# Kernel optimization log

Measured on AMD Instinct MI355X. Metric: run time of the kernel, lower is better.

The kernel has to match this reference:

```python
import jax, jax.numpy as jnp
import numpy as np

HEADS = 8
LANDMARKS = 256
PINV_ITERS = 6
KSZ = 33          # res_conv kernel size (lucidrains default)
LN_EPS = 1e-5


def setup_inputs() -> dict:
    key = jax.random.key(0)
    ks = jax.random.split(key, 5)
    b, n, d = 4, 8192, 512
    inner = 512  # heads * dim_head = 8 * 64
    s = 0.02
    return {
        "x": jax.random.normal(ks[0], (b, n, d), jnp.float32),
        "ln_w": jnp.ones((d,), jnp.float32),
        "ln_b": jnp.zeros((d,), jnp.float32),
        "w_qkv": jax.random.normal(ks[1], (3 * inner, d), jnp.float32) * s,  # Linear(d, 3*inner, bias=False)
        "w_out": jax.random.normal(ks[2], (d, inner), jnp.float32) * s,      # Linear(inner, d)
        "b_out": jnp.zeros((d,), jnp.float32),
        "conv_w": jax.random.normal(ks[3], (HEADS, 1, KSZ, 1), jnp.float32) * 0.1,  # depthwise Conv2d(h,h,(33,1),groups=h)
    }


def _pinv(x, iters):
    # Moore-Penrose iterative pseudo-inverse (lucidrains)
    abs_x = jnp.abs(x)
    scale = jnp.max(abs_x.sum(-1)) * jnp.max(abs_x.sum(-2))
    z = jnp.swapaxes(x, -1, -2) / scale
    I = jnp.eye(x.shape[-1], dtype=x.dtype)
    for _ in range(iters):
        xz = x @ z
        z = 0.25 * z @ (13.0 * I - xz @ (15.0 * I - xz @ (7.0 * I - xz)))
    return z


def _forward(x, ln_w, ln_b, w_qkv, w_out, b_out, conv_w):
    b, n, d = x.shape
    h, m = HEADS, LANDMARKS
    dh = d // h  # 64
    # --- LayerNorm ---
    mu = jnp.mean(x, -1, keepdims=True)
    var = jnp.var(x, -1, keepdims=True)
    xn = (x - mu) / jnp.sqrt(var + LN_EPS) * ln_w + ln_b
    # --- qkv ---
    qkv = xn @ w_qkv.T
    q, k, v = jnp.split(qkv, 3, axis=-1)
    to_heads = lambda t: t.reshape(b, n, h, dh).transpose(0, 2, 1, 3)  # b h n dh
    q = to_heads(q) * (dh ** -0.5)
    k = to_heads(k)
    v = to_heads(v)
    # --- landmarks: mean over contiguous groups of length l (einops '(n l) d -> n d') ---
    l = n // m
    q_l = q.reshape(b, h, m, l, dh).mean(3)  # b h m dh
    k_l = k.reshape(b, h, m, l, dh).mean(3)
    # --- three softmax attention matrices ---
    attn1 = jax.nn.softmax(jnp.einsum('bhid,bhjd->bhij', q, k_l), -1)    # b h n m
    attn2 = jax.nn.softmax(jnp.einsum('bhid,bhjd->bhij', q_l, k_l), -1)  # b h m m
    attn3 = jax.nn.softmax(jnp.einsum('bhid,bhjd->bhij', q_l, k), -1)    # b h m n
    out = (attn1 @ _pinv(attn2, PINV_ITERS)) @ (attn3 @ v)               # b h n dh
    # --- residual depthwise conv over sequence dim, per head, shared over dh ---
    pad = KSZ // 2
    res = jax.lax.conv_general_dilated(
        v, conv_w, window_strides=(1, 1), padding=[(pad, pad), (0, 0)],
        dimension_numbers=('NCHW', 'OIHW', 'NCHW'), feature_group_count=h)
    out = out + res
    out = out.transpose(0, 2, 1, 3).reshape(b, n, h * dh)
    attn_out = out @ w_out.T + b_out  # dropout is identity in eval
    return x + attn_out  # TransLayer residual


def reference(x, ln_w, ln_b, w_qkv, w_out, b_out, conv_w):
    return _forward(x, ln_w, ln_b, w_qkv, w_out, b_out, conv_w)
```

## Files before the change

kernel.cpp:

```cpp
#include <hip/hip_runtime.h>

typedef unsigned short u16;
typedef unsigned int u32;
typedef __attribute__((ext_vector_type(8))) short bf16x8;
typedef __attribute__((ext_vector_type(4))) float f32x4;

__device__ __forceinline__ float bf2f(u16 u) {
    union { u32 i; float f; } z; z.i = ((u32)u) << 16; return z.f;
}
__device__ __forceinline__ float bflo(u32 w) {
    union { u32 i; float f; } z; z.i = w << 16; return z.f;
}
__device__ __forceinline__ float bfhi(u32 w) {
    union { u32 i; float f; } z; z.i = w & 0xffff0000u; return z.f;
}
__device__ __forceinline__ u16 f2bf(float f) {
    union { float f; u32 i; } z; z.f = f;
    u32 x = z.i;
    return (u16)((x + 0x7FFFu + ((x >> 16) & 1u)) >> 16);
}
__device__ __forceinline__ u32 pack2bf(float a, float b) {
    return (u32)f2bf(a) | ((u32)f2bf(b) << 16);
}
template<int BF>
__device__ __forceinline__ float ldin(const void* p, size_t i) {
    return BF ? bf2f(((const u16*)p)[i]) : ((const float*)p)[i];
}


__global__ void detect_dtype(const void* lnw, int* flg) {
    if (threadIdx.x == 0 && blockIdx.x == 0) {
        u32 w = *(const u32*)lnw;
        *flg = (w == 0x3F803F80u) ? 1 : 0;
    }
}

__global__ __launch_bounds__(256) void conv2bf(const void* src, u16* dst, int count, const int* flg) {
    int idx = (blockIdx.x * 256 + threadIdx.x) * 4;
    if (idx >= count) return;
    if (*flg) {
        *(ulonglong1*)&dst[idx] = *(const ulonglong1*)&((const u16*)src)[idx];
    } else {
        const float* s = (const float*)src;
        u32 p0 = pack2bf(s[idx], s[idx + 1]);
        u32 p1 = pack2bf(s[idx + 2], s[idx + 3]);
        *(uint2*)&dst[idx] = make_uint2(p0, p1);
    }
}

template<int BF>
__device__ __forceinline__ void ln_row(const void* x, const void* lnw, const void* lnb, u16* xn) {
    int lane = threadIdx.x & 63;
    size_t row = (size_t)blockIdx.x * 4 + (threadIdx.x >> 6);
    size_t base = row * 512;
    float v[8];
    if (BF) {
        uint4 u = ((const uint4*)((const u16*)x + base))[lane];
        u32 wd[4] = {u.x, u.y, u.z, u.w};
#pragma unroll
        for (int e = 0; e < 4; e++) { v[2 * e] = bflo(wd[e]); v[2 * e + 1] = bfhi(wd[e]); }
    } else {
        const float4* xp = (const float4*)((const float*)x + base) + 2 * lane;
        float4 a = xp[0], b = xp[1];
        v[0] = a.x; v[1] = a.y; v[2] = a.z; v[3] = a.w;
        v[4] = b.x; v[5] = b.y; v[6] = b.z; v[7] = b.w;
    }
    float s = 0.f, s2 = 0.f;
#pragma unroll
    for (int e = 0; e < 8; e++) { s += v[e]; s2 += v[e] * v[e]; }
#pragma unroll
    for (int m = 1; m < 64; m <<= 1) { s += __shfl_xor(s, m); s2 += __shfl_xor(s2, m); }
    float mu = s * (1.f / 512.f);
    float var = s2 * (1.f / 512.f) - mu * mu;
    float rstd = rsqrtf(var + 1e-5f);
    float wv[8], bv[8];
    if (BF) {
        uint4 uw = ((const uint4*)lnw)[lane];
        uint4 ub = ((const uint4*)lnb)[lane];
        u32 ww[4] = {uw.x, uw.y, uw.z, uw.w};
        u32 bb[4] = {ub.x, ub.y, ub.z, ub.w};
#pragma unroll
        for (int e = 0; e < 4; e++) {
            wv[2 * e] = bflo(ww[e]); wv[2 * e + 1] = bfhi(ww[e]);
            bv[2 * e] = bflo(bb[e]); bv[2 * e + 1] = bfhi(bb[e]);
        }
    } else {
        const float4* wp = (const float4*)lnw + 2 * lane;
        const float4* bp = (const float4*)lnb + 2 * lane;
        float4 w0 = wp[0], w1 = wp[1], b0 = bp[0], b1 = bp[1];
        wv[0] = w0.x; wv[1] = w0.y; wv[2] = w0.z; wv[3] = w0.w;
        wv[4] = w1.x; wv[5] = w1.y; wv[6] = w1.z; wv[7] = w1.w;
        bv[0] = b0.x; bv[1] = b0.y; bv[2] = b0.z; bv[3] = b0.w;
        bv[4] = b1.x; bv[5] = b1.y; bv[6] = b1.z; bv[7] = b1.w;
    }
    uint4 o;
    u32 ow[4];
#pragma unroll
    for (int e = 0; e < 4; e++) {
        float f0 = (v[2 * e] - mu) * rstd * wv[2 * e] + bv[2 * e];
        float f1 = (v[2 * e + 1] - mu) * rstd * wv[2 * e + 1] + bv[2 * e + 1];
        ow[e] = pack2bf(f0, f1);
    }
    o.x = ow[0]; o.y = ow[1]; o.z = ow[2]; o.w = ow[3];
    ((uint4*)(xn + base))[lane] = o;
}
__global__ __launch_bounds__(256) void ln_fused(
    const void* x, const void* lnw, const void* lnb, u16* xn, const int* flg) {
    if (*flg) ln_row<1>(x, lnw, lnb, xn);
    else      ln_row<0>(x, lnw, lnb, xn);
}

__global__ __launch_bounds__(256) void mfma_gemm_qkv(
    const u16* __restrict__ A, const u16* __restrict__ B,
    u16* __restrict__ qp, u16* __restrict__ kp, u16* __restrict__ vp)
{
    __shared__ u16 Asl[128][40];
    __shared__ u16 Bsl[128][40];
    int t = threadIdx.x;
    int wave = t >> 6, lane = t & 63;
    int bid = blockIdx.y * 12 + blockIdx.x;
    int w = (bid & 7) * 384 + (bid >> 3);
    int col0 = (w % 12) * 128, row0 = (w / 12) * 128;
    int wr = (wave & 1) * 64, wc = (wave >> 1) * 64;
    int lrow = lane & 15, koff = (lane >> 4) * 8;
    f32x4 acc[4][4] = {};
    int srow = t >> 2, sch = (t & 3) * 8;
    for (int k0 = 0; k0 < 512; k0 += 32) {
        *(float4*)&Asl[srow][sch]      = *(const float4*)&A[(size_t)(row0 + srow) * 512 + k0 + sch];
        *(float4*)&Asl[srow + 64][sch] = *(const float4*)&A[(size_t)(row0 + srow + 64) * 512 + k0 + sch];
        *(float4*)&Bsl[srow][sch]      = *(const float4*)&B[(size_t)(col0 + srow) * 512 + k0 + sch];
        *(float4*)&Bsl[srow + 64][sch] = *(const float4*)&B[(size_t)(col0 + srow + 64) * 512 + k0 + sch];
        __syncthreads();
        bf16x8 af[4], bfr[4];
#pragma unroll
        for (int i = 0; i < 4; i++) af[i]  = *(const bf16x8*)&Asl[wr + 16 * i + lrow][koff];
#pragma unroll
        for (int j = 0; j < 4; j++) bfr[j] = *(const bf16x8*)&Bsl[wc + 16 * j + lrow][koff];
#pragma unroll
        for (int i = 0; i < 4; i++)
#pragma unroll
            for (int j = 0; j < 4; j++)
                acc[i][j] = __builtin_amdgcn_mfma_f32_16x16x32_bf16(af[i], bfr[j], acc[i][j], 0, 0, 0);
        __syncthreads();
    }
    int crow = (lane >> 4) * 4, ccol = lane & 15;
#pragma unroll
    for (int i = 0; i < 4; i++) {
#pragma unroll
        for (int j = 0; j < 4; j++) {
#pragma unroll
            for (int rg = 0; rg < 4; rg++) {
                int row = row0 + wr + 16 * i + crow + rg;
                int col = col0 + wc + 16 * j + ccol;
                int bi = row >> 13, ii = row & 8191;
                int which = col >> 9, wi = col & 511, hh = wi >> 6, cc = wi & 63;
                size_t dst = (((size_t)bi * 8 + hh) * 8192 + ii) * 64 + cc;
                float v = acc[i][j][rg];
                if (which == 0)      qp[dst] = f2bf(v * 0.125f);
                else if (which == 1) kp[dst] = f2bf(v);
                else                 vp[dst] = f2bf(v);
            }
        }
    }
}

__global__ __launch_bounds__(256) void landmark_kernel(
    const u16* __restrict__ q, const u16* __restrict__ k,
    float* __restrict__ q_l, float* __restrict__ k_l,
    u16* __restrict__ q_l_bf, u16* __restrict__ k_l_bf)
{
    int bh = blockIdx.x;
    int g = blockIdx.y * 4 + (threadIdx.x >> 6);
    int c = threadIdx.x & 63;
    const u16* src = blockIdx.z ? k : q;
    float* dst = blockIdx.z ? k_l : q_l;
    u16* dstbf = blockIdx.z ? k_l_bf : q_l_bf;
    const u16* p0 = src + (((size_t)bh * 8192) + (size_t)g * 32) * 64 + c;
    float s = 0.f;
#pragma unroll
    for (int il = 0; il < 32; il++) s += bf2f(p0[(size_t)il * 64]);
    float mean = s * (1.f / 32.f);
    dst[((size_t)bh * 256 + g) * 64 + c] = mean;
    dstbf[((size_t)bh * 256 + g) * 64 + c] = f2bf(mean);
}

__global__ __launch_bounds__(256) void attn2_kernel(
    const float* __restrict__ q_l, const float* __restrict__ k_l, float* __restrict__ attn2)
{
    int bh = blockIdx.x, i = blockIdx.y, j = threadIdx.x;
    __shared__ float qrow[64];
    __shared__ float red[256];
    if (j < 64) qrow[j] = q_l[((size_t)bh * 256 + i) * 64 + j];
    __syncthreads();
    const float* kb = k_l + ((size_t)bh * 256 + j) * 64;
    float s = 0.f;
#pragma unroll
    for (int c = 0; c < 64; c++) s += qrow[c] * kb[c];
    red[j] = s; __syncthreads();
    for (int off = 128; off; off >>= 1) { if (j < off) red[j] = fmaxf(red[j], red[j + off]); __syncthreads(); }
    float mx = red[0]; __syncthreads();
    float e = __expf(s - mx);
    red[j] = e; __syncthreads();
    for (int off = 128; off; off >>= 1) { if (j < off) red[j] += red[j + off]; __syncthreads(); }
    attn2[((size_t)bh * 256 + i) * 256 + j] = e / red[0];
}

__global__ void init_scale(float* s) {
    if (threadIdx.x == 0) { s[0] = 1.0f; s[1] = 0.f; }
}

__global__ __launch_bounds__(256) void colmax_kernel(const float* __restrict__ X, float* __restrict__ scl)
{
    int bh = blockIdx.x, t = threadIdx.x;
    const float* Xb = X + (size_t)bh * 65536;
    float cs = 0.f;
    for (int i = 0; i < 256; i++) cs += fabsf(Xb[(size_t)i * 256 + t]);
    __shared__ float red[256];
    red[t] = cs; __syncthreads();
    for (int off = 128; off; off >>= 1) { if (t < off) red[t] = fmaxf(red[t], red[t + off]); __syncthreads(); }
    if (t == 0) atomicMax((u32*)&scl[1], __float_as_uint(red[0]));
}

__global__ __launch_bounds__(256) void zinit_p(
    const float* __restrict__ X, const float* __restrict__ scl,
    u16* __restrict__ Zh, u16* __restrict__ Zl)
{
    __shared__ float tile[64][65];
    int b = blockIdx.x;
    int j0 = blockIdx.y * 64, i0 = blockIdx.z * 64;
    float s = scl[0] * scl[1];
    const float* Xb = X + (size_t)b * 65536;
    int t = threadIdx.x;
#pragma unroll
    for (int p = 0; p < 16; p++) {
        int idx = t + 256 * p; int jj = idx >> 6, ii = idx & 63;
        tile[jj][ii] = Xb[(size_t)(j0 + jj) * 256 + i0 + ii];
    }
    __syncthreads();
#pragma unroll
    for (int p = 0; p < 16; p++) {
        int idx = t + 256 * p; int ii = idx >> 6, jj = idx & 63;
        float v = tile[jj][ii] / s;
        u16 hi = f2bf(v);
        u16 lo = f2bf(v - bf2f(hi));
        size_t o = ((size_t)b * 256 + i0 + ii) * 256 + j0 + jj;
        Zh[o] = hi; Zl[o] = lo;
    }
}

__global__ __launch_bounds__(256) void split_at2(
    const float* __restrict__ src, u16* __restrict__ dh, u16* __restrict__ dl)
{
    int idx = (blockIdx.x * 256 + threadIdx.x) * 4;
    float4 v = *(const float4*)&src[idx];
    ushort4 h, l;
    h.x = f2bf(v.x); l.x = f2bf(v.x - bf2f(h.x));
    h.y = f2bf(v.y); l.y = f2bf(v.y - bf2f(h.y));
    h.z = f2bf(v.z); l.z = f2bf(v.z - bf2f(h.z));
    h.w = f2bf(v.w); l.w = f2bf(v.w - bf2f(h.w));
    *(ushort4*)&dh[idx] = h;
    *(ushort4*)&dl[idx] = l;
}

__global__ __launch_bounds__(256) void bmm_fused(
    const float* __restrict__ A, const float* __restrict__ B,
    float* __restrict__ C, float* __restrict__ Cneg,
    int N, float alpha, float cdiag)
{
    int batch = blockIdx.x;
    int row0 = blockIdx.y * 64, col0 = blockIdx.z * 64;
    const float* Ab = A + (size_t)batch * 256 * 256;
    const float* Bb = B + (size_t)batch * 256 * N;
    __shared__ float As[32][68];
    __shared__ float Bs[32][68];
    int t = threadIdx.x, tx = t & 15, ty = t >> 4;
    float acc[4][4] = {};
    for (int k0 = 0; k0 < 256; k0 += 32) {
#pragma unroll
        for (int p = 0; p < 8; p++) {
            int idx = t + 256 * p;
            int ra = idx >> 5, ca = idx & 31;
            As[ca][ra] = Ab[(size_t)(row0 + ra) * 256 + k0 + ca];
            int kb = idx >> 6, cb = idx & 63;
            Bs[kb][cb] = Bb[(size_t)(k0 + kb) * N + col0 + cb];
        }
        __syncthreads();
#pragma unroll
        for (int kk = 0; kk < 32; kk++) {
            float4 av = *(const float4*)&As[kk][ty * 4];
            float4 bv = *(const float4*)&Bs[kk][tx * 4];
            float a[4] = {av.x, av.y, av.z, av.w};
            float bb[4] = {bv.x, bv.y, bv.z, bv.w};
#pragma unroll
            for (int i = 0; i < 4; i++)
#pragma unroll
                for (int j = 0; j < 4; j++) acc[i][j] += a[i] * bb[j];
        }
        __syncthreads();
    }
#pragma unroll
    for (int i = 0; i < 4; i++) {
        int row = row0 + ty * 4 + i;
#pragma unroll
        for (int j = 0; j < 4; j++) {
            int col = col0 + tx * 4 + j;
            float v = alpha * acc[i][j];
            size_t idx = (size_t)batch * 256 * N + (size_t)row * N + col;
            if (C)    C[idx] = v;
            if (Cneg) Cneg[idx] = ((row == col) ? cdiag : 0.f) - v;
        }
    }
}

__global__ __launch_bounds__(256) void bmm3p(
    const u16* __restrict__ Ahg, const u16* __restrict__ Alg,
    const u16* __restrict__ Bhg, const u16* __restrict__ Blg,
    u16* __restrict__ Ch, u16* __restrict__ Cl,
    u16* __restrict__ Nh, u16* __restrict__ Nl,
    float* __restrict__ Cf, float alpha, float cdiag)
{
    __shared__ u16 Ah[64][40], Al[64][40], Bh[64][40], Bl[64][40];
    int batch = blockIdx.x;
    int row0 = blockIdx.y * 64, col0 = blockIdx.z * 64;
    size_t boff = (size_t)batch * 65536;
    int t = threadIdx.x, wave = t >> 6, lane = t & 63;
    int lrow = lane & 15, koff = (lane >> 4) * 8;
    int ar = t >> 2, akq = (t & 3) * 8;
    f32x4 acc[4] = {};
    for (int k0 = 0; k0 < 256; k0 += 32) {
        *(uint4*)&Ah[ar][akq] = *(const uint4*)&Ahg[boff + (size_t)(row0 + ar) * 256 + k0 + akq];
        *(uint4*)&Al[ar][akq] = *(const uint4*)&Alg[boff + (size_t)(row0 + ar) * 256 + k0 + akq];
#pragma unroll
        for (int p = 0; p < 2; p++) {
            int c = t + 256 * p; int n = c & 63, kq = (c >> 6) * 4;
            size_t bb = boff + (size_t)(k0 + kq) * 256 + col0 + n;
            ushort4 hv, lv;
            hv.x = Bhg[bb];       lv.x = Blg[bb];
            hv.y = Bhg[bb + 256]; lv.y = Blg[bb + 256];
            hv.z = Bhg[bb + 512]; lv.z = Blg[bb + 512];
            hv.w = Bhg[bb + 768]; lv.w = Blg[bb + 768];
            *(ushort4*)&Bh[n][kq] = hv;
            *(ushort4*)&Bl[n][kq] = lv;
        }
        __syncthreads();
        bf16x8 ah = *(const bf16x8*)&Ah[wave * 16 + lrow][koff];
        bf16x8 al = *(const bf16x8*)&Al[wave * 16 + lrow][koff];
#pragma unroll
        for (int j = 0; j < 4; j++) {
            bf16x8 bhv = *(const bf16x8*)&Bh[16 * j + lrow][koff];
            bf16x8 blv = *(const bf16x8*)&Bl[16 * j + lrow][koff];
            acc[j] = __builtin_amdgcn_mfma_f32_16x16x32_bf16(ah, bhv, acc[j], 0, 0, 0);
            acc[j] = __builtin_amdgcn_mfma_f32_16x16x32_bf16(ah, blv, acc[j], 0, 0, 0);
            acc[j] = __builtin_amdgcn_mfma_f32_16x16x32_bf16(al, bhv, acc[j], 0, 0, 0);
        }
        __syncthreads();
    }
    int crow = (lane >> 4) * 4, ccol = lane & 15;
#pragma unroll
    for (int j = 0; j < 4; j++) {
#pragma unroll
        for (int r = 0; r < 4; r++) {
            int row = row0 + wave * 16 + crow + r;
            int col = col0 + 16 * j + ccol;
            float v = alpha * acc[j][r];
            size_t idx = boff + (size_t)row * 256 + col;
            if (Cf) Cf[idx] = v;
            if (Ch) {
                u16 hi = f2bf(v);
                Ch[idx] = hi; Cl[idx] = f2bf(v - bf2f(hi));
            }
            if (Nh) {
                float w = ((row == col) ? cdiag : 0.f) - v;
                u16 hi = f2bf(w);
                Nh[idx] = hi; Nl[idx] = f2bf(w - bf2f(hi));
            }
        }
    }
}

__global__ __launch_bounds__(256) void t2bf(const float* __restrict__ src, u16* __restrict__ dst)
{
    __shared__ u16 tile[256][72];
    int bh = blockIdx.x, t = threadIdx.x;
    const float* s = src + (size_t)bh * 16384;
    u16* d = dst + (size_t)bh * 16384;
#pragma unroll
    for (int p = 0; p < 64; p++) {
        int idx = t + 256 * p;
        tile[idx >> 6][idx & 63] = f2bf(s[idx]);
    }
    __syncthreads();
#pragma unroll
    for (int p = 0; p < 64; p++) {
        int o = t + 256 * p;
        int n = o >> 8, kk = o & 255;
        d[o] = tile[kk][n];
    }
}

__global__ __launch_bounds__(256) void attn3v_mfma(
    const u16* __restrict__ qlbf, const u16* __restrict__ k, const u16* __restrict__ v,
    float* __restrict__ Opart, float* __restrict__ lpart)
{
    __shared__ __align__(16) char smem[8192 + 8192 + 9216];
    char* QsB = smem;
    char* KsB = smem + 8192;
    char* VtB = smem + 16384;

    int bh = blockIdx.x, rb = blockIdx.y, seg = blockIdx.z;
    int t = threadIdx.x;
    int w = t >> 6, lane = t & 63, cl = lane & 15, kg = lane >> 4;
    int wrow = w * 16;

    {
        const uint4* qg = (const uint4*)(qlbf + ((size_t)bh * 256 + rb * 64) * 64);
#pragma unroll
        for (int p = 0; p < 2; p++) {
            int c = t + 256 * p; int row = c >> 3, cc = c & 7;
            *(uint4*)(QsB + row * 128 + ((cc * 16) ^ ((row & 7) << 4))) = qg[c];
        }
    }
    __syncthreads();
    bf16x8 af0, af1;
    {
        int row = wrow + cl, sw = (row & 7) << 4;
        af0 = *(const bf16x8*)(QsB + row * 128 + ((kg * 16) ^ sw));
        af1 = *(const bf16x8*)(QsB + row * 128 + ((kg * 16 + 64) ^ sw));
    }

    const uint4* kb4 = (const uint4*)(k + (size_t)bh * 8192 * 64);
    const uint4* vb4 = (const uint4*)(v + (size_t)bh * 8192 * 64);

    int krow = t >> 3, kcc = t & 7;
    int pn = t >> 3, vcc = t & 7;

    f32x4 acc_o[4] = {};
    float rsum[4] = {0.f, 0.f, 0.f, 0.f};

    int n0 = seg * 2048;
    uint4 kr0 = kb4[(size_t)(n0 + krow) * 8 + kcc];
    uint4 kr1 = kb4[(size_t)(n0 + krow + 32) * 8 + kcc];
    uint4 va  = vb4[(size_t)(n0 + 2 * pn) * 8 + vcc];
    uint4 vbv = vb4[(size_t)(n0 + 2 * pn + 1) * 8 + vcc];

    for (int ti = 0; ti < 32; ti++) {
        __syncthreads();
        *(uint4*)(KsB + krow * 128 + ((kcc * 16) ^ ((krow & 7) << 4))) = kr0;
        {
            int row = krow + 32;
            *(uint4*)(KsB + row * 128 + ((kcc * 16) ^ ((row & 7) << 4))) = kr1;
        }
        {
            u32 aw[4] = {va.x, va.y, va.z, va.w};
            u32 bw[4] = {vbv.x, vbv.y, vbv.z, vbv.w};
            int colb = pn * 4;
#pragma unroll
            for (int e = 0; e < 8; e++) {
                u32 avv = (aw[e >> 1] >> ((e & 1) * 16)) & 0xffffu;
                u32 bvv = (bw[e >> 1] >> ((e & 1) * 16)) & 0xffffu;
                int row = vcc * 8 + e;
                *(u32*)(VtB + row * 144 + (colb ^ ((row & 0x38) << 1))) = avv | (bvv << 16);
            }
        }
        __syncthreads();
        if (ti < 31) {
            int nn = n0 + (ti + 1) * 64;
            kr0 = kb4[(size_t)(nn + krow) * 8 + kcc];
            kr1 = kb4[(size_t)(nn + krow + 32) * 8 + kcc];
            va  = vb4[(size_t)(nn + 2 * pn) * 8 + vcc];
            vbv = vb4[(size_t)(nn + 2 * pn + 1) * 8 + vcc];
        }
        f32x4 s[4] = {};
#pragma unroll
        for (int j = 0; j < 4; j++) {
            int row = 16 * j + cl, sw = (row & 7) << 4;
            bf16x8 b0 = *(const bf16x8*)(KsB + row * 128 + ((kg * 16) ^ sw));
            bf16x8 b1 = *(const bf16x8*)(KsB + row * 128 + ((kg * 16 + 64) ^ sw));
            s[j] = __builtin_amdgcn_mfma_f32_16x16x32_bf16(af0, b0, s[j], 0, 0, 0);
            s[j] = __builtin_amdgcn_mfma_f32_16x16x32_bf16(af1, b1, s[j], 0, 0, 0);
        }
#pragma unroll
        for (int j = 0; j < 4; j++)
#pragma unroll
            for (int r = 0; r < 4; r++) {
                float e = __expf(s[j][r]);
                s[j][r] = e;
                rsum[r] += e;
            }
#pragma unroll
        for (int j = 0; j < 4; j++) {
#pragma unroll
            for (int r = 0; r < 4; r++) {
                float pv = s[j][r];
                float po = __shfl_xor(pv, 1);
                if (!(cl & 1)) {
                    int row = wrow + kg * 4 + r;
                    int col = 16 * j + cl;
                    *(u32*)(QsB + row * 128 + ((col * 2) ^ ((row & 7) << 4))) = pack2bf(pv, po);
                }
            }
        }
        {
            int prow = wrow + cl, psw = (prow & 7) << 4;
            bf16x8 pa0 = *(const bf16x8*)(QsB + prow * 128 + ((kg * 16) ^ psw));
            bf16x8 pa1 = *(const bf16x8*)(QsB + prow * 128 + ((kg * 16 + 64) ^ psw));
#pragma unroll
            for (int j = 0; j < 4; j++) {
                int vr = 16 * j + cl;
                int vsw = (vr & 0x38) << 1;
                bf16x8 vb0 = *(const bf16x8*)(VtB + vr * 144 + ((kg * 16) ^ vsw));
                bf16x8 vb1 = *(const bf16x8*)(VtB + vr * 144 + ((kg * 16 + 64) ^ vsw));
                acc_o[j] = __builtin_amdgcn_mfma_f32_16x16x32_bf16(pa0, vb0, acc_o[j], 0, 0, 0);
                acc_o[j] = __builtin_amdgcn_mfma_f32_16x16x32_bf16(pa1, vb1, acc_o[j], 0, 0, 0);
            }
        }
    }
#pragma unroll
    for (int j = 0; j < 4; j++)
#pragma unroll
        for (int r = 0; r < 4; r++) {
            int lm = rb * 64 + wrow + kg * 4 + r;
            Opart[(((size_t)(bh * 256 + lm)) * 4 + seg) * 64 + 16 * j + cl] = acc_o[j][r];
        }
#pragma unroll
    for (int m = 1; m < 16; m <<= 1)
#pragma unroll
        for (int r = 0; r < 4; r++) rsum[r] += __shfl_xor(rsum[r], m);
    if (cl == 0) {
#pragma unroll
        for (int r = 0; r < 4; r++)
            lpart[((size_t)(bh * 256 + rb * 64 + wrow + kg * 4 + r)) * 4 + seg] = rsum[r];
    }
}

__global__ __launch_bounds__(256) void merge3(
    const float* __restrict__ Opart, const float* __restrict__ lpart, float* __restrict__ w3v)
{
    size_t idx = (size_t)blockIdx.x * 256 + threadIdx.x;
    size_t row = idx >> 6; int c = (int)(idx & 63);
    float l = lpart[row * 4] + lpart[row * 4 + 1] + lpart[row * 4 + 2] + lpart[row * 4 + 3];
    float ov = 0.f;
#pragma unroll
    for (int s = 0; s < 4; s++) ov += Opart[(row * 4 + s) * 64 + c];
    w3v[idx] = ov / l;
}

__global__ __launch_bounds__(256) void attn1_out_mfma(
    const u16* __restrict__ q, const u16* __restrict__ klbf,
    const u16* __restrict__ tmatT, const u16* __restrict__ v,
    const void* __restrict__ conv_w, u16* __restrict__ out2, const int* flg)
{
    __shared__ __align__(16) char smem[31296];
    char* QsB = smem;
    char* KsB = smem + 8192;
    char* TsB = smem + 16384;
    float* Osm = (float*)smem;
    char* VsB = smem + 17472;
    __shared__ float cw[33];

    int bh = blockIdx.x, rb = blockIdx.y;
    int bi = bh >> 3, h = bh & 7;
    int r0 = rb * 64;
    int t = threadIdx.x;
    int w = t >> 6, lane = t & 63, cl = lane & 15, kg = lane >> 4;
    int wrow = w * 16;

    {
        const uint4* qg = (const uint4*)(q + ((size_t)bh * 8192 + r0) * 64);
#pragma unroll
        for (int p = 0; p < 2; p++) {
            int c = t + 256 * p; int row = c >> 3, cc = c & 7;
            *(uint4*)(QsB + row * 128 + ((cc * 16) ^ ((row & 7) << 4))) = qg[c];
        }
    }
    if (t < 33) cw[t] = (*flg) ? bf2f(((const u16*)conv_w)[h * 33 + t])
                               : ((const float*)conv_w)[h * 33 + t];
    __syncthreads();

    bf16x8 af0, af1;
    {
        int row = wrow + cl, sw = (row & 7) << 4;
        af0 = *(const bf16x8*)(QsB + row * 128 + ((kg * 16) ^ sw));
        af1 = *(const bf16x8*)(QsB + row * 128 + ((kg * 16 + 64) ^ sw));
    }

    const uint4* klg = (const uint4*)(klbf + (size_t)bh * 16384);
    const uint4* tg  = (const uint4*)(tmatT + (size_t)bh * 16384);

    f32x4 accO[4] = {};
    float rsum[4] = {0.f, 0.f, 0.f, 0.f};

    for (int lc = 0; lc < 4; lc++) {
        __syncthreads();
#pragma unroll
        for (int p = 0; p < 2; p++) {
            int c = t + 256 * p; int row = c >> 3, cc = c & 7;
            *(uint4*)(KsB + row * 128 + ((cc * 16) ^ ((row & 7) << 4))) = klg[(size_t)(lc * 64 + row) * 8 + cc];
        }
#pragma unroll
        for (int p = 0; p < 2; p++) {
            int c = t + 256 * p; int n = c >> 3, cc = c & 7;
            *(uint4*)(TsB + n * 128 + ((cc * 16) ^ ((n & 7) << 4))) = tg[(size_t)n * 32 + lc * 8 + cc];
        }
        __syncthreads();
        f32x4 s[4] = {};
#pragma unroll
        for (int j = 0; j < 4; j++) {
            int row = 16 * j + cl, sw = (row & 7) << 4;
            bf16x8 b0 = *(const bf16x8*)(KsB + row * 128 + ((kg * 16) ^ sw));
            bf16x8 b1 = *(const bf16x8*)(KsB + row * 128 + ((kg * 16 + 64) ^ sw));
            s[j] = __builtin_amdgcn_mfma_f32_16x16x32_bf16(af0, b0, s[j], 0, 0, 0);
            s[j] = __builtin_amdgcn_mfma_f32_16x16x32_bf16(af1, b1, s[j], 0, 0, 0);
        }
#pragma unroll
        for (int j = 0; j < 4; j++)
#pragma unroll
            for (int r = 0; r < 4; r++) {
                float e = __expf(s[j][r]);
                s[j][r] = e;
                rsum[r] += e;
            }
#pragma unroll
        for (int j = 0; j < 4; j++) {
#pragma unroll
            for (int r = 0; r < 4; r++) {
                float pv = s[j][r];
                float po = __shfl_xor(pv, 1);
                if (!(cl & 1)) {
                    int row = wrow + kg * 4 + r;
                    int col = 16 * j + cl;
                    *(u32*)(QsB + row * 128 + ((col * 2) ^ ((row & 7) << 4))) = pack2bf(pv, po);
                }
            }
        }
        {
            int prow = wrow + cl, psw = (prow & 7) << 4;
            bf16x8 pa0 = *(const bf16x8*)(QsB + prow * 128 + ((kg * 16) ^ psw));
            bf16x8 pa1 = *(const bf16x8*)(QsB + prow * 128 + ((kg * 16 + 64) ^ psw));
#pragma unroll
            for (int j = 0; j < 4; j++) {
                int n = 16 * j + cl, tsw = (n & 7) << 4;
                bf16x8 b0 = *(const bf16x8*)(TsB + n * 128 + ((kg * 16) ^ tsw));
                bf16x8 b1 = *(const bf16x8*)(TsB + n * 128 + ((kg * 16 + 64) ^ tsw));
                accO[j] = __builtin_amdgcn_mfma_f32_16x16x32_bf16(pa0, b0, accO[j], 0, 0, 0);
                accO[j] = __builtin_amdgcn_mfma_f32_16x16x32_bf16(pa1, b1, accO[j], 0, 0, 0);
            }
        }
    }
#pragma unroll
    for (int m = 1; m < 16; m <<= 1)
#pragma unroll
        for (int r = 0; r < 4; r++) rsum[r] += __shfl_xor(rsum[r], m);
    float linv[4];
#pragma unroll
    for (int r = 0; r < 4; r++) linv[r] = 1.f / rsum[r];
#pragma unroll
    for (int j = 0; j < 4; j++)
#pragma unroll
        for (int r = 0; r < 4; r++) accO[j][r] *= linv[r];

    __syncthreads();
    uint4 vreg[3];
    {
        const uint4* vg = (const uint4*)(v + (size_t)bh * 8192 * 64);
#pragma unroll
        for (int p = 0; p < 3; p++) {
            int c = t + 256 * p; int vr = c >> 3, cc = c & 7;
            int gr = r0 - 16 + vr;
            vreg[p] = (gr >= 0 && gr < 8192) ? vg[(size_t)gr * 8 + cc] : make_uint4(0, 0, 0, 0);
        }
    }
#pragma unroll
    for (int j = 0; j < 4; j++)
#pragma unroll
        for (int r = 0; r < 4; r++)
            Osm[(wrow + kg * 4 + r) * 68 + 16 * j + cl] = accO[j][r];
#pragma unroll
    for (int p = 0; p < 3; p++) {
        int c = t + 256 * p; int vr = c >> 3, cc = c & 7;
        *(uint4*)(VsB + vr * 144 + cc * 16) = vreg[p];
    }
    __syncthreads();
    float cwr[33];
#pragma unroll
    for (int i = 0; i < 33; i++) cwr[i] = cw[i];
    int rgrp = t >> 4, cchunk = t & 15;
    float racc[4][4] = {};
#pragma unroll
    for (int vri = 0; vri < 36; vri++) {
        int vr = rgrp * 4 + vri;
        uint2 vv = *(const uint2*)(VsB + vr * 144 + cchunk * 8);
        float v0 = bflo(vv.x), v1 = bfhi(vv.x), v2 = bflo(vv.y), v3 = bfhi(vv.y);
#pragma unroll
        for (int rr = 0; rr < 4; rr++) {
            int tap = vri - rr;
            if (tap >= 0 && tap < 33) {
                float cwt = cwr[tap];
                racc[rr][0] += cwt * v0;
                racc[rr][1] += cwt * v1;
                racc[rr][2] += cwt * v2;
                racc[rr][3] += cwt * v3;
            }
        }
    }
#pragma unroll
    for (int rr = 0; rr < 4; rr++) {
        int ro = rgrp * 4 + rr;
        float4 ov = *(const float4*)&Osm[ro * 68 + cchunk * 4];
        float f0 = ov.x + racc[rr][0];
        float f1 = ov.y + racc[rr][1];
        float f2 = ov.z + racc[rr][2];
        float f3 = ov.w + racc[rr][3];
        size_t base = ((size_t)bi * 8192 + r0 + ro) * 512 + h * 64 + cchunk * 4;
        *(uint2*)(out2 + base) = make_uint2(pack2bf(f0, f1), pack2bf(f2, f3));
    }
}

__global__ __launch_bounds__(256) void mfma_gemm_out(
    const u16* __restrict__ A, const u16* __restrict__ B,
    const void* __restrict__ bias, const void* __restrict__ x,
    void* __restrict__ out, const int* flg)
{
    __shared__ u16 Asl[128][40];
    __shared__ u16 Bsl[128][40];
    int t = threadIdx.x;
    int wave = t >> 6, lane = t & 63;
    int bid = blockIdx.y * 4 + blockIdx.x;
    int w = (bid & 7) * 128 + (bid >> 3);
    int col0 = (w & 3) * 128, row0 = (w >> 2) * 128;
    int wr = (wave & 1) * 64, wc = (wave >> 1) * 64;
    int lrow = lane & 15, koff = (lane >> 4) * 8;
    f32x4 acc[4][4] = {};
    int srow = t >> 2, sch = (t & 3) * 8;
    for (int k0 = 0; k0 < 512; k0 += 32) {
        *(float4*)&Asl[srow][sch]      = *(const float4*)&A[(size_t)(row0 + srow) * 512 + k0 + sch];
        *(float4*)&Asl[srow + 64][sch] = *(const float4*)&A[(size_t)(row0 + srow + 64) * 512 + k0 + sch];
        *(float4*)&Bsl[srow][sch]      = *(const float4*)&B[(size_t)(col0 + srow) * 512 + k0 + sch];
        *(float4*)&Bsl[srow + 64][sch] = *(const float4*)&B[(size_t)(col0 + srow + 64) * 512 + k0 + sch];
        __syncthreads();
        bf16x8 af[4], bfr[4];
#pragma unroll
        for (int i = 0; i < 4; i++) af[i]  = *(const bf16x8*)&Asl[wr + 16 * i + lrow][koff];
#pragma unroll
        for (int j = 0; j < 4; j++) bfr[j] = *(const bf16x8*)&Bsl[wc + 16 * j + lrow][koff];
#pragma unroll
        for (int i = 0; i < 4; i++)
#pragma unroll
            for (int j = 0; j < 4; j++)
                acc[i][j] = __builtin_amdgcn_mfma_f32_16x16x32_bf16(af[i], bfr[j], acc[i][j], 0, 0, 0);
        __syncthreads();
    }
    int crow = (lane >> 4) * 4, ccol = lane & 15;
    int isbf = *flg;
#pragma unroll
    for (int i = 0; i < 4; i++) {
#pragma unroll
        for (int j = 0; j < 4; j++) {
#pragma unroll
            for (int rg = 0; rg < 4; rg++) {
                int row = row0 + wr + 16 * i + crow + rg;
                int col = col0 + wc + 16 * j + ccol;
                size_t idx = (size_t)row * 512 + col;
                float bv = isbf ? bf2f(((const u16*)bias)[col]) : ((const float*)bias)[col];
                float xv = isbf ? bf2f(((const u16*)x)[idx]) : ((const float*)x)[idx];
                float v = acc[i][j][rg] + bv + xv;
                if (isbf) ((u16*)out)[idx] = f2bf(v);
                else      ((float*)out)[idx] = v;
            }
        }
    }
}

extern "C" void kernel_launch(void* const* d_in, const int* in_sizes, int n_in,
                              void* d_out, int out_size, void* d_ws, size_t ws_size,
                              hipStream_t stream) {
    const void* x      = d_in[0];
    const void* ln_w   = d_in[1];
    const void* ln_b   = d_in[2];
    const void* w_qkv  = d_in[3];
    const void* w_out  = d_in[4];
    const void* b_out  = d_in[5];
    const void* conv_w = d_in[6];

    char* base = (char*)d_ws;
    size_t off = 0;
    auto alloc = [&](size_t nbytes) { char* p = base + off; off += (nbytes + 255) & ~size_t(255); return p; };
    u16*   q_bf  = (u16*)  alloc(16777216ull * 2);
    u16*   k_bf  = (u16*)  alloc(16777216ull * 2);
    u16*   v_bf  = (u16*)  alloc(16777216ull * 2);
    u16*   xn_bf = (u16*)  alloc(16777216ull * 2);
    u16*   wq_bf = (u16*)  alloc(786432ull * 2);
    u16*   wo_bf = (u16*)  alloc(262144ull * 2);
    float* q_l   = (float*)alloc(524288ull * 4);
    float* k_l   = (float*)alloc(524288ull * 4);
    float* at2   = (float*)alloc(2097152ull * 4);
    float* zf32  = (float*)alloc(2097152ull * 4);
    float* Zb    = (float*)alloc(2097152ull * 4);
    float* XZ    = (float*)alloc(2097152ull * 4);
    u16*   T1h   = (u16*)  alloc(2097152ull * 2);
    u16*   T1l   = (u16*)  alloc(2097152ull * 2);
    float* w3v   = (float*)alloc(524288ull * 4);
    float* tmat  = (float*)alloc(524288ull * 4);
    u16*   ql_bf = (u16*)  alloc(524288ull * 2);
    u16*   kl_bf = (u16*)  alloc(524288ull * 2);
    u16*   tmT   = (u16*)  alloc(524288ull * 2);
    float* scl   = (float*)alloc(256);
    int*   flg   = (int*)  alloc(256);

    u16* a2h = xn_bf;
    u16* a2l = xn_bf + 2097152ull;
    u16* Zah = xn_bf + 2097152ull * 2;
    u16* Zal = xn_bf + 2097152ull * 3;
    u16* Zbh = xn_bf + 2097152ull * 4;
    u16* Zbl = xn_bf + 2097152ull * 5;
    u16* XZh = xn_bf + 2097152ull * 6;
    u16* XZl = xn_bf + 2097152ull * 7;

    detect_dtype<<<1, 64, 0, stream>>>(ln_w, flg);
    ln_fused<<<8192, 256, 0, stream>>>(x, ln_w, ln_b, xn_bf, flg);
    conv2bf<<<768, 256, 0, stream>>>(w_qkv, wq_bf, 786432, flg);
    conv2bf<<<256, 256, 0, stream>>>(w_out, wo_bf, 262144, flg);
    mfma_gemm_qkv<<<dim3(12, 256), 256, 0, stream>>>(xn_bf, wq_bf, q_bf, k_bf, v_bf);
    landmark_kernel<<<dim3(32, 64, 2), 256, 0, stream>>>(q_bf, k_bf, q_l, k_l, ql_bf, kl_bf);
    attn2_kernel<<<dim3(32, 256), 256, 0, stream>>>(q_l, k_l, at2);
    init_scale<<<1, 64, 0, stream>>>(scl);
    colmax_kernel<<<32, 256, 0, stream>>>(at2, scl);
    zinit_p<<<dim3(32, 4, 4), 256, 0, stream>>>(at2, scl, Zah, Zal);
    split_at2<<<2048, 256, 0, stream>>>(at2, a2h, a2l);

    u16 *zch = Zah, *zcl = Zal, *znh = Zbh, *znl = Zbl;
    for (int it = 0; it < 6; it++) {
        bmm3p<<<dim3(32, 4, 4), 256, 0, stream>>>(a2h, a2l, zch, zcl, XZh, XZl, T1h, T1l, nullptr, 1.f, 7.f);
        bmm3p<<<dim3(32, 4, 4), 256, 0, stream>>>(XZh, XZl, T1h, T1l, nullptr, nullptr, znh, znl, nullptr, 1.f, 15.f);
        bmm3p<<<dim3(32, 4, 4), 256, 0, stream>>>(XZh, XZl, znh, znl, nullptr, nullptr, T1h, T1l, nullptr, 1.f, 13.f);
        bmm3p<<<dim3(32, 4, 4), 256, 0, stream>>>(zch, zcl, T1h, T1l, znh, znl, nullptr, nullptr,
                                                  (it == 5) ? zf32 : nullptr, 0.25f, 0.f);
        u16* th = zch; zch = znh; znh = th;
        u16* tl = zcl; zcl = znl; znl = tl;
    }
    float* Opart = Zb;
    float* lpart = XZ;

    attn3v_mfma<<<dim3(32, 4, 4), 256, 0, stream>>>(ql_bf, k_bf, v_bf, Opart, lpart);
    merge3<<<2048, 256, 0, stream>>>(Opart, lpart, w3v);
    bmm_fused<<<dim3(32, 4, 1), 256, 0, stream>>>(zf32, w3v, tmat, nullptr, 64, 1.f, 0.f);
    t2bf<<<32, 256, 0, stream>>>(tmat, tmT);
    u16* out2 = k_bf;
    attn1_out_mfma<<<dim3(32, 128), 256, 0, stream>>>(q_bf, kl_bf, tmT, v_bf, conv_w, out2, flg);
    mfma_gemm_out<<<dim3(4, 256), 256, 0, stream>>>(out2, wo_bf, b_out, x, d_out, flg);
}
```

Before: 868.4 us.

## Load full landmark K and T tiles once and remap bmm3p block order

attn1_out_mfma now loads all 256 landmark keys and the full transposed T matrix into 64KB of shared memory in one pass, computes the whole 64x256 score tile in registers, normalizes, then runs one P·T pass. This replaces the four-chunk loop with a barrier pair per chunk. Q fragments are read straight from global memory rather than staged through shared memory. Separately, bmm3p remaps its flat block index so tiles of the same batch are spread across blocks in interleaved order. The 64KB of LDS and 16 accumulator tiles per thread raise register and LDS pressure, which may cut occupancy.

```diff
diff --git a/kernel.cpp b/kernel.cpp
--- a/kernel.cpp
+++ b/kernel.cpp
@@ -320,8 +320,11 @@
     float* __restrict__ Cf, float alpha, float cdiag)
 {
     __shared__ u16 Ah[64][40], Al[64][40], Bh[64][40], Bl[64][40];
-    int batch = blockIdx.x;
-    int row0 = blockIdx.y * 64, col0 = blockIdx.z * 64;
+    int bid = blockIdx.x + 32 * (blockIdx.y + 4 * blockIdx.z);
+    int w = (bid & 7) * 64 + (bid >> 3);
+    int batch = w >> 4;
+    int tile = w & 15;
+    int row0 = (tile >> 2) * 64, col0 = (tile & 3) * 64;
     size_t boff = (size_t)batch * 65536;
     int t = threadIdx.x, wave = t >> 6, lane = t & 63;
     int lrow = lane & 15, koff = (lane >> 4) * 8;
@@ -370,9 +373,9 @@
                 Ch[idx] = hi; Cl[idx] = f2bf(v - bf2f(hi));
             }
             if (Nh) {
-                float w = ((row == col) ? cdiag : 0.f) - v;
-                u16 hi = f2bf(w);
-                Nh[idx] = hi; Nl[idx] = f2bf(w - bf2f(hi));
+                float w2 = ((row == col) ? cdiag : 0.f) - v;
+                u16 hi = f2bf(w2);
+                Nh[idx] = hi; Nl[idx] = f2bf(w2 - bf2f(hi));
             }
         }
     }
@@ -550,13 +553,12 @@
     const u16* __restrict__ tmatT, const u16* __restrict__ v,
     const void* __restrict__ conv_w, u16* __restrict__ out2, const int* flg)
 {
-    __shared__ __align__(16) char smem[31296];
-    char* QsB = smem;
-    char* KsB = smem + 8192;
-    char* TsB = smem + 16384;
+    __shared__ __align__(16) char smem[65536];
+    char* KsB = smem;
+    char* TsB = smem + 32768;
     float* Osm = (float*)smem;
     char* VsB = smem + 17472;
-    __shared__ float cw[33];
+    float* cwp = (float*)(smem + 31360);
 
     int bh = blockIdx.x, rb = blockIdx.y;
     int bi = bh >> 3, h = bh & 7;
@@ -565,101 +567,85 @@
     int w = t >> 6, lane = t & 63, cl = lane & 15, kg = lane >> 4;
     int wrow = w * 16;
 
-    {
-        const uint4* qg = (const uint4*)(q + ((size_t)bh * 8192 + r0) * 64);
-#pragma unroll
-        for (int p = 0; p < 2; p++) {
-            int c = t + 256 * p; int row = c >> 3, cc = c & 7;
-            *(uint4*)(QsB + row * 128 + ((cc * 16) ^ ((row & 7) << 4))) = qg[c];
-        }
-    }
-    if (t < 33) cw[t] = (*flg) ? bf2f(((const u16*)conv_w)[h * 33 + t])
-                               : ((const float*)conv_w)[h * 33 + t];
-    __syncthreads();
-
     bf16x8 af0, af1;
     {
-        int row = wrow + cl, sw = (row & 7) << 4;
-        af0 = *(const bf16x8*)(QsB + row * 128 + ((kg * 16) ^ sw));
-        af1 = *(const bf16x8*)(QsB + row * 128 + ((kg * 16 + 64) ^ sw));
-    }
-
-    const uint4* klg = (const uint4*)(klbf + (size_t)bh * 16384);
-    const uint4* tg  = (const uint4*)(tmatT + (size_t)bh * 16384);
-
+        const u16* qr = q + ((size_t)bh * 8192 + r0 + wrow + cl) * 64 + kg * 8;
+        af0 = *(const bf16x8*)qr;
+        af1 = *(const bf16x8*)(qr + 32);
+    }
+    {
+        const uint4* klg = (const uint4*)(klbf + (size_t)bh * 16384);
+#pragma unroll
+        for (int p = 0; p < 8; p++) {
+            int c = t + 256 * p; int row = c >> 3, cc = c & 7;
+            *(uint4*)(KsB + row * 128 + ((cc * 16) ^ ((row & 7) << 4))) = klg[c];
+        }
+        const uint4* tg = (const uint4*)(tmatT + (size_t)bh * 16384);
+#pragma unroll
+        for (int p = 0; p < 8; p++) {
+            int c = t + 256 * p; int n = c >> 5, cc = c & 31;
+            *(uint4*)(TsB + n * 512 + ((cc * 16) ^ ((n & 7) << 4))) = tg[c];
+        }
+    }
+    __syncthreads();
+
+    f32x4 acc1[16] = {};
+#pragma unroll
+    for (int j = 0; j < 16; j++) {
+        int row = 16 * j + cl, sw = (row & 7) << 4;
+        bf16x8 b0 = *(const bf16x8*)(KsB + row * 128 + ((kg * 16) ^ sw));
+        bf16x8 b1 = *(const bf16x8*)(KsB + row * 128 + ((kg * 16 + 64) ^ sw));
+        acc1[j] = __builtin_amdgcn_mfma_f32_16x16x32_bf16(af0, b0, acc1[j], 0, 0, 0);
+        acc1[j] = __builtin_amdgcn_mfma_f32_16x16x32_bf16(af1, b1, acc1[j], 0, 0, 0);
+    }
+    float rsum[4] = {0.f, 0.f, 0.f, 0.f};
+#pragma unroll
+    for (int j = 0; j < 16; j++)
+#pragma unroll
+        for (int r = 0; r < 4; r++) {
+            float e = __expf(acc1[j][r]);
+            acc1[j][r] = e;
+            rsum[r] += e;
+        }
+#pragma unroll
+    for (int m = 1; m < 16; m <<= 1)
+#pragma unroll
+        for (int r = 0; r < 4; r++) rsum[r] += __shfl_xor(rsum[r], m);
+    float linv[4];
+#pragma unroll
+    for (int r = 0; r < 4; r++) linv[r] = 1.f / rsum[r];
+
+    __syncthreads();
+
+#pragma unroll
+    for (int j = 0; j < 16; j++) {
+#pragma unroll
+        for (int r = 0; r < 4; r++) {
+            float pv = acc1[j][r] * linv[r];
+            float po = __shfl_xor(pv, 1);
+            if (!(cl & 1)) {
+                int row = wrow + kg * 4 + r;
+                int col = 16 * j + cl;
+                *(u32*)(KsB + row * 512 + ((col * 2) ^ ((row & 7) << 4))) = pack2bf(pv, po);
+            }
+        }
+    }
     f32x4 accO[4] = {};
-    float rsum[4] = {0.f, 0.f, 0.f, 0.f};
-
-    for (int lc = 0; lc < 4; lc++) {
-        __syncthreads();
-#pragma unroll
-        for (int p = 0; p < 2; p++) {
-            int c = t + 256 * p; int row = c >> 3, cc = c & 7;
-            *(uint4*)(KsB + row * 128 + ((cc * 16) ^ ((row & 7) << 4))) = klg[(size_t)(lc * 64 + row) * 8 + cc];
-        }
-#pragma unroll
-        for (int p = 0; p < 2; p++) {
-            int c = t + 256 * p; int n = c >> 3, cc = c & 7;
-            *(uint4*)(TsB + n * 128 + ((cc * 16) ^ ((n & 7) << 4))) = tg[(size_t)n * 32 + lc * 8 + cc];
-        }
-        __syncthreads();
-        f32x4 s[4] = {};
-#pragma unroll
-        for (int j = 0; j < 4; j++) {
-            int row = 16 * j + cl, sw = (row & 7) << 4;
-            bf16x8 b0 = *(const bf16x8*)(KsB + row * 128 + ((kg * 16) ^ sw));
-            bf16x8 b1 = *(const bf16x8*)(KsB + row * 128 + ((kg * 16 + 64) ^ sw));
-            s[j] = __builtin_amdgcn_mfma_f32_16x16x32_bf16(af0, b0, s[j], 0, 0, 0);
-            s[j] = __builtin_amdgcn_mfma_f32_16x16x32_bf16(af1, b1, s[j], 0, 0, 0);
-        }
-#pragma unroll
-        for (int j = 0; j < 4; j++)
-#pragma unroll
-            for (int r = 0; r < 4; r++) {
-                float e = __expf(s[j][r]);
-                s[j][r] = e;
-                rsum[r] += e;
-            }
-#pragma unroll
-        for (int j = 0; j < 4; j++) {
-#pragma unroll
-            for (int r = 0; r < 4; r++) {
-                float pv = s[j][r];
-                float po = __shfl_xor(pv, 1);
-                if (!(cl & 1)) {
-                    int row = wrow + kg * 4 + r;
-                    int col = 16 * j + cl;
-                    *(u32*)(QsB + row * 128 + ((col * 2) ^ ((row & 7) << 4))) = pack2bf(pv, po);
-                }
-            }
-        }
-        {
-            int prow = wrow + cl, psw = (prow & 7) << 4;
-            bf16x8 pa0 = *(const bf16x8*)(QsB + prow * 128 + ((kg * 16) ^ psw));
-            bf16x8 pa1 = *(const bf16x8*)(QsB + prow * 128 + ((kg * 16 + 64) ^ psw));
+    {
+        int prow = wrow + cl, psw = (prow & 7) << 4;
+#pragma unroll
+        for (int ks = 0; ks < 8; ks++) {
+            bf16x8 pa = *(const bf16x8*)(KsB + prow * 512 + ((kg * 16 + ks * 64) ^ psw));
 #pragma unroll
             for (int j = 0; j < 4; j++) {
                 int n = 16 * j + cl, tsw = (n & 7) << 4;
-                bf16x8 b0 = *(const bf16x8*)(TsB + n * 128 + ((kg * 16) ^ tsw));
-                bf16x8 b1 = *(const bf16x8*)(TsB + n * 128 + ((kg * 16 + 64) ^ tsw));
-                accO[j] = __builtin_amdgcn_mfma_f32_16x16x32_bf16(pa0, b0, accO[j], 0, 0, 0);
-                accO[j] = __builtin_amdgcn_mfma_f32_16x16x32_bf16(pa1, b1, accO[j], 0, 0, 0);
-            }
-        }
-    }
-#pragma unroll
-    for (int m = 1; m < 16; m <<= 1)
-#pragma unroll
-        for (int r = 0; r < 4; r++) rsum[r] += __shfl_xor(rsum[r], m);
-    float linv[4];
-#pragma unroll
-    for (int r = 0; r < 4; r++) linv[r] = 1.f / rsum[r];
-#pragma unroll
-    for (int j = 0; j < 4; j++)
-#pragma unroll
-        for (int r = 0; r < 4; r++) accO[j][r] *= linv[r];
-
+                bf16x8 bb = *(const bf16x8*)(TsB + n * 512 + ((kg * 16 + ks * 64) ^ tsw));
+                accO[j] = __builtin_amdgcn_mfma_f32_16x16x32_bf16(pa, bb, accO[j], 0, 0, 0);
+            }
+        }
+    }
     __syncthreads();
+
     uint4 vreg[3];
     {
         const uint4* vg = (const uint4*)(v + (size_t)bh * 8192 * 64);
@@ -670,6 +656,8 @@
             vreg[p] = (gr >= 0 && gr < 8192) ? vg[(size_t)gr * 8 + cc] : make_uint4(0, 0, 0, 0);
         }
     }
+    if (t < 33) cwp[t] = (*flg) ? bf2f(((const u16*)conv_w)[h * 33 + t])
+                                : ((const float*)conv_w)[h * 33 + t];
 #pragma unroll
     for (int j = 0; j < 4; j++)
 #pragma unroll
@@ -683,7 +671,7 @@
     __syncthreads();
     float cwr[33];
 #pragma unroll
-    for (int i = 0; i < 33; i++) cwr[i] = cw[i];
+    for (int i = 0; i < 33; i++) cwr[i] = cwp[i];
     int rgrp = t >> 4, cchunk = t & 15;
     float racc[4][4] = {};
 #pragma unroll
```

Measured after the change: 894.3 us. 3.0% more time.
